# Kernel tuning notes

Measured on AMD Instinct MI355X. Metric: run time of the kernel, lower is better.

Reference implementation:

```python
import jax, jax.numpy as jnp
import numpy as np

TK, HA = 3, 8          # num_blocks, num_heads
AVGF = 32              # num_submatrices
LN_EPS = 1e-5


def _layernorm(x, g, b):
    m = jnp.mean(x, axis=-1, keepdims=True)
    v = jnp.mean((x - m) ** 2, axis=-1, keepdims=True)
    return (x - m) / jnp.sqrt(v + LN_EPS) * g + b


def setup_inputs() -> dict:
    key = jax.random.key(0)
    ks = jax.random.split(key, 12)
    A, B, T = 16, 128, 512
    M = A * B              # 2048
    Dh = M // HA           # 256
    H = 4 * M              # 8192
    s = 0.05               # scale randn params so activations stay finite
    return {
        "x": jax.random.normal(ks[0], (A, B, T), jnp.float32),
        "weight": jax.random.normal(ks[1], (M, M), jnp.float32) * s,
        "Wq": jax.random.normal(ks[2], (TK, HA, Dh, M), jnp.float32) * s,
        "Wk": jax.random.normal(ks[3], (TK, HA, Dh, M), jnp.float32) * s,
        "Wv": jax.random.normal(ks[4], (TK, HA, Dh, M), jnp.float32) * s,
        "Wo": jax.random.normal(ks[5], (TK, M, M), jnp.float32) * s,
        "ln1_g": jnp.ones((M,), jnp.float32),
        "ln1_b": jnp.zeros((M,), jnp.float32),
        "ln2_g": jnp.ones((M,), jnp.float32),
        "ln2_b": jnp.zeros((M,), jnp.float32),
        "fc1_w": jax.random.normal(ks[6], (H, M), jnp.float32) * 0.02,
        "fc1_b": jnp.zeros((H,), jnp.float32),
        "fc2_w": jax.random.normal(ks[7], (M, H), jnp.float32) * 0.02,
        "fc2_b": jnp.zeros((M,), jnp.float32),
    }


def reference(x, weight, Wq, Wk, Wv, Wo, ln1_g, ln1_b, ln2_g, ln2_b,
              fc1_w, fc1_b, fc2_w, fc2_b):
    A, B, T = x.shape
    M = A * B
    Dh = M // HA
    seg = T // AVGF
    # redefine(): transpose(0,2) -> (T,B,A), segment-average along time, flatten
    xt = jnp.transpose(x, (2, 1, 0))                       # (T, B, A)
    xc = xt.reshape(AVGF, seg, B, A).mean(axis=1)          # (AVGF, B, A)
    xcf = xc.reshape(AVGF, M)                              # (AVGF, M)
    # savespace[i] = weight @ x[i]  + sinusoidal positional bias
    pos = jnp.arange(AVGF, dtype=jnp.float32)[:, None]
    je = jnp.arange(0, M, 2, dtype=jnp.float32)
    ang = pos / (10000.0 ** (2.0 * je / M))                # (AVGF, M/2)
    bias = jnp.zeros((AVGF, M), jnp.float32)
    bias = bias.at[:, 0::2].set(jnp.sin(ang)).at[:, 1::2].set(jnp.cos(ang))
    s0 = xcf @ weight.T + bias                             # (AVGF, M)
    scale = 1.0 / jnp.sqrt(jnp.float32(Dh))

    # Sequential recurrence over tokens: vcum[a] carries the cumulative
    # softmax-weighted V sum (softmax over a scalar == 1) per block/head.
    def step(vcum, s):
        for a in range(TK):
            xn = _layernorm(s, ln1_g, ln1_b)
            q = jnp.einsum('hdm,m->hd', Wq[a], xn)         # (HA, Dh)
            k = jnp.einsum('hdm,m->hd', Wk[a], xn)
            v = jnp.einsum('hdm,m->hd', Wv[a], xn)
            scores = jnp.sum(q * k, axis=-1) * scale       # (HA,) scalars
            w = jax.nn.softmax(scores[:, None], axis=-1)[:, 0]  # ones
            vcum = vcum.at[a].add(w[:, None] * v)
            s = Wo[a] @ vcum[a].reshape(-1) + s
            s = _layernorm(s, ln2_g, ln2_b) + s
            h = jax.nn.gelu(fc1_w @ s + fc1_b, approximate=False)
            s = fc2_w @ h + fc2_b
        return vcum, s

    vcum0 = jnp.zeros((TK, HA, Dh), s0.dtype)
    _, out = jax.lax.scan(step, vcum0, s0)                 # (AVGF, M)
    return out.reshape(AVGF, B, A)
```

## Files before the change

kernel.cpp:

```cpp
#include <hip/hip_runtime.h>
#include <hip/hip_bf16.h>
#include <math.h>

typedef __attribute__((ext_vector_type(8))) short short8;
typedef __attribute__((ext_vector_type(4))) float floatx4;

__device__ inline unsigned f2bf1(float f) {
    union { float f; unsigned u; } v; v.f = f;
    return (v.u + 0x8000u) >> 16;
}

__device__ inline short8 pack8(float4 a, float4 b) {
    short8 r;
    r[0] = (short)f2bf1(a.x); r[1] = (short)f2bf1(a.y);
    r[2] = (short)f2bf1(a.z); r[3] = (short)f2bf1(a.w);
    r[4] = (short)f2bf1(b.x); r[5] = (short)f2bf1(b.y);
    r[6] = (short)f2bf1(b.z); r[7] = (short)f2bf1(b.w);
    return r;
}

__global__ __launch_bounds__(128) void avg_k(const float* __restrict__ x,
                                             float* __restrict__ xcf) {
    int blk = blockIdx.x;
    int a = blk >> 7, b = blk & 127;
    int t = threadIdx.x;
    const float4 v = *(const float4*)(x + ((size_t)a * 128 + b) * 512 + t * 4);
    float s = v.x + v.y + v.z + v.w;
    s += __shfl_xor(s, 1);
    s += __shfl_xor(s, 2);
    if ((t & 3) == 0) {
        int seg = t >> 2;
        xcf[seg * 2048 + b * 16 + a] = s * (1.0f / 16.0f);
    }
}

__global__ __launch_bounds__(256) void ln_k(const float* __restrict__ Sin,
                                            const float* __restrict__ g,
                                            const float* __restrict__ b,
                                            float* __restrict__ out, int addres) {
    __shared__ float red[8];
    const int row = blockIdx.x, t = threadIdx.x;
    const float* xr = Sin + (size_t)row * 2048;
    float4 v0 = *(const float4*)(xr + t * 4);
    float4 v1 = *(const float4*)(xr + 1024 + t * 4);
    float s = v0.x + v0.y + v0.z + v0.w + v1.x + v1.y + v1.z + v1.w;
    for (int o = 32; o; o >>= 1) s += __shfl_down(s, o);
    if ((t & 63) == 0) red[t >> 6] = s;
    __syncthreads();
    float mean = (red[0] + red[1] + red[2] + red[3]) * (1.0f / 2048.0f);
    float d0 = v0.x - mean, d1 = v0.y - mean, d2 = v0.z - mean, d3 = v0.w - mean;
    float e0 = v1.x - mean, e1 = v1.y - mean, e2 = v1.z - mean, e3 = v1.w - mean;
    float s2 = d0*d0 + d1*d1 + d2*d2 + d3*d3 + e0*e0 + e1*e1 + e2*e2 + e3*e3;
    for (int o = 32; o; o >>= 1) s2 += __shfl_down(s2, o);
    if ((t & 63) == 0) red[4 + (t >> 6)] = s2;
    __syncthreads();
    float var = (red[4] + red[5] + red[6] + red[7]) * (1.0f / 2048.0f);
    float rs = 1.0f / sqrtf(var + 1e-5f);
    float4 g0 = *(const float4*)(g + t * 4);
    float4 g1 = *(const float4*)(g + 1024 + t * 4);
    float4 b0 = *(const float4*)(b + t * 4);
    float4 b1 = *(const float4*)(b + 1024 + t * 4);
    float4 o0, o1;
    o0.x = d0 * rs * g0.x + b0.x; o0.y = d1 * rs * g0.y + b0.y;
    o0.z = d2 * rs * g0.z + b0.z; o0.w = d3 * rs * g0.w + b0.w;
    o1.x = e0 * rs * g1.x + b1.x; o1.y = e1 * rs * g1.y + b1.y;
    o1.z = e2 * rs * g1.z + b1.z; o1.w = e3 * rs * g1.w + b1.w;
    if (addres) {
        o0.x += v0.x; o0.y += v0.y; o0.z += v0.z; o0.w += v0.w;
        o1.x += v1.x; o1.y += v1.y; o1.z += v1.z; o1.w += v1.w;
    }
    *(float4*)(out + (size_t)row * 2048 + t * 4) = o0;
    *(float4*)(out + (size_t)row * 2048 + 1024 + t * 4) = o1;
}

__global__ __launch_bounds__(256) void cumsum_k(float* __restrict__ V) {
    int c = blockIdx.x * 256 + threadIdx.x;
    float run = 0.f;
#pragma unroll
    for (int i = 0; i < 32; i++) { run += V[i * 2048 + c]; V[i * 2048 + c] = run; }
}

__global__ __launch_bounds__(256) void gelu_k(float* __restrict__ H,
                                              const float* __restrict__ b1) {
    int idx4 = blockIdx.x * 256 + threadIdx.x;
    int col4 = idx4 & 2047;
    float4 v = *(const float4*)(H + (size_t)idx4 * 4);
    const float4 bb = *(const float4*)(b1 + col4 * 4);
    v.x += bb.x; v.y += bb.y; v.z += bb.z; v.w += bb.w;
    v.x = 0.5f * v.x * (1.0f + erff(v.x * 0.70710678118654752f));
    v.y = 0.5f * v.y * (1.0f + erff(v.y * 0.70710678118654752f));
    v.z = 0.5f * v.z * (1.0f + erff(v.z * 0.70710678118654752f));
    v.w = 0.5f * v.w * (1.0f + erff(v.w * 0.70710678118654752f));
    *(float4*)(H + (size_t)idx4 * 4) = v;
}

template<int KCHUNK, int MODE>
__global__ __launch_bounds__(256) void gemm_k(const float* __restrict__ X,
                                              const float* __restrict__ W,
                                              float* __restrict__ C,
                                              const float* __restrict__ bias,
                                              int N, int K) {
    constexpr int PITCH = KCHUNK + 8;
    __shared__ unsigned short Xs[32 * PITCH];
    const int tid = threadIdx.x;
    const int bx = blockIdx.x, by = blockIdx.y;
    const int kb0 = by * KCHUNK;

    constexpr int NF4 = 32 * (KCHUNK / 4);
    for (int f = tid; f < NF4; f += 256) {
        int row = f / (KCHUNK / 4), c4 = f % (KCHUNK / 4);
        const float4 v = *(const float4*)(X + (size_t)row * K + kb0 + c4 * 4);
        ushort4 p;
        p.x = (unsigned short)f2bf1(v.x);
        p.y = (unsigned short)f2bf1(v.y);
        p.z = (unsigned short)f2bf1(v.z);
        p.w = (unsigned short)f2bf1(v.w);
        *(ushort4*)&Xs[row * PITCH + c4 * 4] = p;
    }
    __syncthreads();

    const int w = tid >> 6, lane = tid & 63;
    const int q = lane >> 4, r16 = lane & 15;
    const int nb = bx * 128 + w * 32;
    floatx4 acc[2][2] = {};
    const float* wp0 = W + (size_t)(nb + r16) * K + kb0 + q * 8;
    const float* wp1 = W + (size_t)(nb + 16 + r16) * K + kb0 + q * 8;

#pragma unroll
    for (int kk = 0; kk < KCHUNK; kk += 32) {
        short8 a0 = *(const short8*)&Xs[r16 * PITCH + kk + q * 8];
        short8 a1 = *(const short8*)&Xs[(16 + r16) * PITCH + kk + q * 8];
        {
            float4 u0 = *(const float4*)(wp0 + kk);
            float4 u1 = *(const float4*)(wp0 + kk + 4);
            short8 bf = pack8(u0, u1);
            acc[0][0] = __builtin_amdgcn_mfma_f32_16x16x32_bf16(a0, bf, acc[0][0], 0, 0, 0);
            acc[1][0] = __builtin_amdgcn_mfma_f32_16x16x32_bf16(a1, bf, acc[1][0], 0, 0, 0);
        }
        {
            float4 u0 = *(const float4*)(wp1 + kk);
            float4 u1 = *(const float4*)(wp1 + kk + 4);
            short8 bf = pack8(u0, u1);
            acc[0][1] = __builtin_amdgcn_mfma_f32_16x16x32_bf16(a0, bf, acc[0][1], 0, 0, 0);
            acc[1][1] = __builtin_amdgcn_mfma_f32_16x16x32_bf16(a1, bf, acc[1][1], 0, 0, 0);
        }
    }

#pragma unroll
    for (int mt = 0; mt < 2; mt++)
#pragma unroll
        for (int nt = 0; nt < 2; nt++)
#pragma unroll
            for (int e = 0; e < 4; e++) {
                int i = mt * 16 + q * 4 + e;
                int n = nb + nt * 16 + r16;
                float v = acc[mt][nt][e];
                if (MODE == 1 && by == 0) v += bias[n];
                if (MODE == 2 && by == 0) {
                    int ne = n & ~1;
                    float ang = (float)i * __expf(-(float)ne * (9.210340371976184f / 1024.0f));
                    v += (n & 1) ? cosf(ang) : sinf(ang);
                }
                atomicAdd(C + (size_t)i * N + n, v);
            }
}

extern "C" void kernel_launch(void* const* d_in, const int* in_sizes, int n_in,
                              void* d_out, int out_size, void* d_ws, size_t ws_size,
                              hipStream_t stream) {
    const float* x      = (const float*)d_in[0];
    const float* weight = (const float*)d_in[1];
    const float* Wv     = (const float*)d_in[4];
    const float* Wo     = (const float*)d_in[5];
    const float* ln1g   = (const float*)d_in[6];
    const float* ln1b   = (const float*)d_in[7];
    const float* ln2g   = (const float*)d_in[8];
    const float* ln2b   = (const float*)d_in[9];
    const float* fc1w   = (const float*)d_in[10];
    const float* fc1b   = (const float*)d_in[11];
    const float* fc2w   = (const float*)d_in[12];
    const float* fc2b   = (const float*)d_in[13];
    float* ws  = (float*)d_ws;
    float* xcf = ws;
    float* S   = ws + 65536;
    float* Xn  = ws + 131072;
    float* V   = ws + 196608;
    float* H   = ws + 262144;
    float* out = (float*)d_out;

    avg_k<<<2048, 128, 0, stream>>>(x, xcf);

    hipMemsetAsync(S, 0, 65536 * 4, stream);
    gemm_k<128, 2><<<dim3(16, 16), 256, 0, stream>>>(xcf, weight, S, nullptr, 2048, 2048);

    for (int a = 0; a < 3; a++) {
        ln_k<<<32, 256, 0, stream>>>(S, ln1g, ln1b, Xn, 0);
        hipMemsetAsync(V, 0, 65536 * 4, stream);
        gemm_k<128, 0><<<dim3(16, 16), 256, 0, stream>>>(Xn, Wv + (size_t)a * 4194304, V, nullptr, 2048, 2048);
        cumsum_k<<<8, 256, 0, stream>>>(V);
        gemm_k<128, 0><<<dim3(16, 16), 256, 0, stream>>>(V, Wo + (size_t)a * 4194304, S, nullptr, 2048, 2048);
        ln_k<<<32, 256, 0, stream>>>(S, ln2g, ln2b, S, 1);
        hipMemsetAsync(H, 0, 262144 * 4, stream);
        gemm_k<256, 0><<<dim3(64, 8), 256, 0, stream>>>(S, fc1w, H, nullptr, 8192, 2048);
        gelu_k<<<256, 256, 0, stream>>>(H, fc1b);
        float* Co = (a == 2) ? out : S;
        hipMemsetAsync(Co, 0, 65536 * 4, stream);
        gemm_k<256, 1><<<dim3(16, 32), 256, 0, stream>>>(H, fc2w, Co, fc2b, 2048, 8192);
    }
}
```

Baseline: 494.7 us.

## Replace atomic split-K accumulation with slab partials and fused reduction epilogues

Split-K GEMMs now write their partial tiles to a per-K-chunk slab with plain stores instead of atomicAdd into memset buffers. Dedicated reduction kernels sum the partials and fuse the following elementwise work: positional bias with LN1, cumsum, residual with LN2, bias with GELU, and bias with the next block's LN1. This removes the memsets, the atomic contention, and the separate ln/cumsum/gelu passes. The cost is extra slab traffic and reduction reads, and the 2048x2048 GEMMs move to finer K-chunks (64), which doubles the split count.

Result: slower. 505.1 us (+2.1%).

```diff
diff --git a/kernel.cpp b/kernel.cpp
--- a/kernel.cpp
+++ b/kernel.cpp
@@ -34,71 +34,10 @@
     }
 }
 
-__global__ __launch_bounds__(256) void ln_k(const float* __restrict__ Sin,
-                                            const float* __restrict__ g,
-                                            const float* __restrict__ b,
-                                            float* __restrict__ out, int addres) {
-    __shared__ float red[8];
-    const int row = blockIdx.x, t = threadIdx.x;
-    const float* xr = Sin + (size_t)row * 2048;
-    float4 v0 = *(const float4*)(xr + t * 4);
-    float4 v1 = *(const float4*)(xr + 1024 + t * 4);
-    float s = v0.x + v0.y + v0.z + v0.w + v1.x + v1.y + v1.z + v1.w;
-    for (int o = 32; o; o >>= 1) s += __shfl_down(s, o);
-    if ((t & 63) == 0) red[t >> 6] = s;
-    __syncthreads();
-    float mean = (red[0] + red[1] + red[2] + red[3]) * (1.0f / 2048.0f);
-    float d0 = v0.x - mean, d1 = v0.y - mean, d2 = v0.z - mean, d3 = v0.w - mean;
-    float e0 = v1.x - mean, e1 = v1.y - mean, e2 = v1.z - mean, e3 = v1.w - mean;
-    float s2 = d0*d0 + d1*d1 + d2*d2 + d3*d3 + e0*e0 + e1*e1 + e2*e2 + e3*e3;
-    for (int o = 32; o; o >>= 1) s2 += __shfl_down(s2, o);
-    if ((t & 63) == 0) red[4 + (t >> 6)] = s2;
-    __syncthreads();
-    float var = (red[4] + red[5] + red[6] + red[7]) * (1.0f / 2048.0f);
-    float rs = 1.0f / sqrtf(var + 1e-5f);
-    float4 g0 = *(const float4*)(g + t * 4);
-    float4 g1 = *(const float4*)(g + 1024 + t * 4);
-    float4 b0 = *(const float4*)(b + t * 4);
-    float4 b1 = *(const float4*)(b + 1024 + t * 4);
-    float4 o0, o1;
-    o0.x = d0 * rs * g0.x + b0.x; o0.y = d1 * rs * g0.y + b0.y;
-    o0.z = d2 * rs * g0.z + b0.z; o0.w = d3 * rs * g0.w + b0.w;
-    o1.x = e0 * rs * g1.x + b1.x; o1.y = e1 * rs * g1.y + b1.y;
-    o1.z = e2 * rs * g1.z + b1.z; o1.w = e3 * rs * g1.w + b1.w;
-    if (addres) {
-        o0.x += v0.x; o0.y += v0.y; o0.z += v0.z; o0.w += v0.w;
-        o1.x += v1.x; o1.y += v1.y; o1.z += v1.z; o1.w += v1.w;
-    }
-    *(float4*)(out + (size_t)row * 2048 + t * 4) = o0;
-    *(float4*)(out + (size_t)row * 2048 + 1024 + t * 4) = o1;
-}
-
-__global__ __launch_bounds__(256) void cumsum_k(float* __restrict__ V) {
-    int c = blockIdx.x * 256 + threadIdx.x;
-    float run = 0.f;
-#pragma unroll
-    for (int i = 0; i < 32; i++) { run += V[i * 2048 + c]; V[i * 2048 + c] = run; }
-}
-
-__global__ __launch_bounds__(256) void gelu_k(float* __restrict__ H,
-                                              const float* __restrict__ b1) {
-    int idx4 = blockIdx.x * 256 + threadIdx.x;
-    int col4 = idx4 & 2047;
-    float4 v = *(const float4*)(H + (size_t)idx4 * 4);
-    const float4 bb = *(const float4*)(b1 + col4 * 4);
-    v.x += bb.x; v.y += bb.y; v.z += bb.z; v.w += bb.w;
-    v.x = 0.5f * v.x * (1.0f + erff(v.x * 0.70710678118654752f));
-    v.y = 0.5f * v.y * (1.0f + erff(v.y * 0.70710678118654752f));
-    v.z = 0.5f * v.z * (1.0f + erff(v.z * 0.70710678118654752f));
-    v.w = 0.5f * v.w * (1.0f + erff(v.w * 0.70710678118654752f));
-    *(float4*)(H + (size_t)idx4 * 4) = v;
-}
-
-template<int KCHUNK, int MODE>
+template<int KCHUNK>
 __global__ __launch_bounds__(256) void gemm_k(const float* __restrict__ X,
                                               const float* __restrict__ W,
-                                              float* __restrict__ C,
-                                              const float* __restrict__ bias,
+                                              float* __restrict__ slab,
                                               int N, int K) {
     constexpr int PITCH = KCHUNK + 8;
     __shared__ unsigned short Xs[32 * PITCH];
@@ -107,6 +46,7 @@
     const int kb0 = by * KCHUNK;
 
     constexpr int NF4 = 32 * (KCHUNK / 4);
+#pragma unroll
     for (int f = tid; f < NF4; f += 256) {
         int row = f / (KCHUNK / 4), c4 = f % (KCHUNK / 4);
         const float4 v = *(const float4*)(X + (size_t)row * K + kb0 + c4 * 4);
@@ -146,6 +86,7 @@
         }
     }
 
+    float* outp = slab + (size_t)by * 32 * N;
 #pragma unroll
     for (int mt = 0; mt < 2; mt++)
 #pragma unroll
@@ -154,15 +95,183 @@
             for (int e = 0; e < 4; e++) {
                 int i = mt * 16 + q * 4 + e;
                 int n = nb + nt * 16 + r16;
-                float v = acc[mt][nt][e];
-                if (MODE == 1 && by == 0) v += bias[n];
-                if (MODE == 2 && by == 0) {
-                    int ne = n & ~1;
-                    float ang = (float)i * __expf(-(float)ne * (9.210340371976184f / 1024.0f));
-                    v += (n & 1) ? cosf(ang) : sinf(ang);
-                }
-                atomicAdd(C + (size_t)i * N + n, v);
+                outp[(size_t)i * N + n] = acc[mt][nt][e];
             }
+}
+
+template<int NCH>
+__device__ inline float4 csum4(const float* __restrict__ slab, size_t stride, size_t off) {
+    float4 a; a.x = 0.f; a.y = 0.f; a.z = 0.f; a.w = 0.f;
+#pragma unroll 8
+    for (int c = 0; c < NCH; c++) {
+        const float4 v = *(const float4*)(slab + (size_t)c * stride + off);
+        a.x += v.x; a.y += v.y; a.z += v.z; a.w += v.w;
+    }
+    return a;
+}
+
+__device__ inline float block_sum(float v, float* red, int t) {
+    for (int o = 32; o; o >>= 1) v += __shfl_down(v, o);
+    if ((t & 63) == 0) red[t >> 6] = v;
+    __syncthreads();
+    float r = red[0] + red[1] + red[2] + red[3];
+    __syncthreads();
+    return r;
+}
+
+#define KEXP (-9.210340371976184f / 1024.0f)
+
+__global__ __launch_bounds__(256) void rW_k(const float* __restrict__ slab,
+                                            const float* __restrict__ g,
+                                            const float* __restrict__ bl,
+                                            float* __restrict__ S,
+                                            float* __restrict__ Xn) {
+    __shared__ float red[4];
+    const int row = blockIdx.x, t = threadIdx.x;
+    const size_t off0 = (size_t)row * 2048 + t * 4, off1 = off0 + 1024;
+    float4 v0 = csum4<32>(slab, 65536, off0);
+    float4 v1 = csum4<32>(slab, 65536, off1);
+    const float fr = (float)row;
+    const int c0 = t * 4, c1 = c0 + 1024;
+    float a0 = fr * __expf((float)c0 * KEXP);
+    float a1 = fr * __expf((float)(c0 + 2) * KEXP);
+    float a2 = fr * __expf((float)c1 * KEXP);
+    float a3 = fr * __expf((float)(c1 + 2) * KEXP);
+    v0.x += sinf(a0); v0.y += cosf(a0); v0.z += sinf(a1); v0.w += cosf(a1);
+    v1.x += sinf(a2); v1.y += cosf(a2); v1.z += sinf(a3); v1.w += cosf(a3);
+    *(float4*)(S + off0) = v0;
+    *(float4*)(S + off1) = v1;
+    float s = v0.x + v0.y + v0.z + v0.w + v1.x + v1.y + v1.z + v1.w;
+    float mean = block_sum(s, red, t) * (1.0f / 2048.0f);
+    float d0 = v0.x - mean, d1 = v0.y - mean, d2 = v0.z - mean, d3 = v0.w - mean;
+    float e0 = v1.x - mean, e1 = v1.y - mean, e2 = v1.z - mean, e3 = v1.w - mean;
+    float s2 = d0*d0 + d1*d1 + d2*d2 + d3*d3 + e0*e0 + e1*e1 + e2*e2 + e3*e3;
+    float var = block_sum(s2, red, t) * (1.0f / 2048.0f);
+    float rs = 1.0f / sqrtf(var + 1e-5f);
+    float4 g0 = *(const float4*)(g + c0), g1 = *(const float4*)(g + c1);
+    float4 b0 = *(const float4*)(bl + c0), b1 = *(const float4*)(bl + c1);
+    float4 o0, o1;
+    o0.x = d0 * rs * g0.x + b0.x; o0.y = d1 * rs * g0.y + b0.y;
+    o0.z = d2 * rs * g0.z + b0.z; o0.w = d3 * rs * g0.w + b0.w;
+    o1.x = e0 * rs * g1.x + b1.x; o1.y = e1 * rs * g1.y + b1.y;
+    o1.z = e2 * rs * g1.z + b1.z; o1.w = e3 * rs * g1.w + b1.w;
+    *(float4*)(Xn + off0) = o0;
+    *(float4*)(Xn + off1) = o1;
+}
+
+__global__ __launch_bounds__(256) void rVcum_k(const float* __restrict__ slab,
+                                               float* __restrict__ Vc) {
+    __shared__ float lds[32 * 64];
+    const int b = blockIdx.x, t = threadIdx.x;
+    {
+        int row = t >> 4, c4 = t & 15;
+        size_t off = (size_t)row * 2048 + b * 64 + c4 * 4;
+        float4 v = csum4<32>(slab, 65536, off);
+        *(float4*)&lds[row * 64 + c4 * 4] = v;
+    }
+    {
+        int row = (t >> 4) + 16, c4 = t & 15;
+        size_t off = (size_t)row * 2048 + b * 64 + c4 * 4;
+        float4 v = csum4<32>(slab, 65536, off);
+        *(float4*)&lds[row * 64 + c4 * 4] = v;
+    }
+    __syncthreads();
+    if (t < 64) {
+        float run = 0.f;
+#pragma unroll
+        for (int i = 0; i < 32; i++) {
+            run += lds[i * 64 + t];
+            Vc[(size_t)i * 2048 + b * 64 + t] = run;
+        }
+    }
+}
+
+__global__ __launch_bounds__(256) void rO_k(const float* __restrict__ slab,
+                                            const float* __restrict__ S,
+                                            const float* __restrict__ g,
+                                            const float* __restrict__ bl,
+                                            float* __restrict__ S2) {
+    __shared__ float red[4];
+    const int row = blockIdx.x, t = threadIdx.x;
+    const size_t off0 = (size_t)row * 2048 + t * 4, off1 = off0 + 1024;
+    float4 v0 = csum4<32>(slab, 65536, off0);
+    float4 v1 = csum4<32>(slab, 65536, off1);
+    const float4 s0 = *(const float4*)(S + off0);
+    const float4 s1 = *(const float4*)(S + off1);
+    v0.x += s0.x; v0.y += s0.y; v0.z += s0.z; v0.w += s0.w;
+    v1.x += s1.x; v1.y += s1.y; v1.z += s1.z; v1.w += s1.w;
+    float s = v0.x + v0.y + v0.z + v0.w + v1.x + v1.y + v1.z + v1.w;
+    float mean = block_sum(s, red, t) * (1.0f / 2048.0f);
+    float d0 = v0.x - mean, d1 = v0.y - mean, d2 = v0.z - mean, d3 = v0.w - mean;
+    float e0 = v1.x - mean, e1 = v1.y - mean, e2 = v1.z - mean, e3 = v1.w - mean;
+    float s2 = d0*d0 + d1*d1 + d2*d2 + d3*d3 + e0*e0 + e1*e1 + e2*e2 + e3*e3;
+    float var = block_sum(s2, red, t) * (1.0f / 2048.0f);
+    float rs = 1.0f / sqrtf(var + 1e-5f);
+    const int c0 = t * 4, c1 = c0 + 1024;
+    float4 g0 = *(const float4*)(g + c0), g1 = *(const float4*)(g + c1);
+    float4 b0 = *(const float4*)(bl + c0), b1 = *(const float4*)(bl + c1);
+    float4 o0, o1;
+    o0.x = d0 * rs * g0.x + b0.x + v0.x; o0.y = d1 * rs * g0.y + b0.y + v0.y;
+    o0.z = d2 * rs * g0.z + b0.z + v0.z; o0.w = d3 * rs * g0.w + b0.w + v0.w;
+    o1.x = e0 * rs * g1.x + b1.x + v1.x; o1.y = e1 * rs * g1.y + b1.y + v1.y;
+    o1.z = e2 * rs * g1.z + b1.z + v1.z; o1.w = e3 * rs * g1.w + b1.w + v1.w;
+    *(float4*)(S2 + off0) = o0;
+    *(float4*)(S2 + off1) = o1;
+}
+
+__global__ __launch_bounds__(256) void rFC1_k(const float* __restrict__ slab,
+                                              const float* __restrict__ bias,
+                                              float* __restrict__ Hb) {
+    const int row = blockIdx.x, t = threadIdx.x;
+#pragma unroll
+    for (int j = 0; j < 8; j++) {
+        const int c4 = t + 256 * j;
+        const size_t off = (size_t)row * 8192 + c4 * 4;
+        float4 v = csum4<8>(slab, 262144, off);
+        const float4 bb = *(const float4*)(bias + c4 * 4);
+        v.x += bb.x; v.y += bb.y; v.z += bb.z; v.w += bb.w;
+        v.x = 0.5f * v.x * (1.0f + erff(v.x * 0.70710678118654752f));
+        v.y = 0.5f * v.y * (1.0f + erff(v.y * 0.70710678118654752f));
+        v.z = 0.5f * v.z * (1.0f + erff(v.z * 0.70710678118654752f));
+        v.w = 0.5f * v.w * (1.0f + erff(v.w * 0.70710678118654752f));
+        *(float4*)(Hb + off) = v;
+    }
+}
+
+__global__ __launch_bounds__(256) void rFC2_k(const float* __restrict__ slab,
+                                              const float* __restrict__ bias,
+                                              float* __restrict__ Sdst,
+                                              float* __restrict__ Xn,
+                                              const float* __restrict__ g,
+                                              const float* __restrict__ bl) {
+    __shared__ float red[4];
+    const int row = blockIdx.x, t = threadIdx.x;
+    const size_t off0 = (size_t)row * 2048 + t * 4, off1 = off0 + 1024;
+    const int c0 = t * 4, c1 = c0 + 1024;
+    float4 v0 = csum4<32>(slab, 65536, off0);
+    float4 v1 = csum4<32>(slab, 65536, off1);
+    const float4 bb0 = *(const float4*)(bias + c0);
+    const float4 bb1 = *(const float4*)(bias + c1);
+    v0.x += bb0.x; v0.y += bb0.y; v0.z += bb0.z; v0.w += bb0.w;
+    v1.x += bb1.x; v1.y += bb1.y; v1.z += bb1.z; v1.w += bb1.w;
+    *(float4*)(Sdst + off0) = v0;
+    *(float4*)(Sdst + off1) = v1;
+    float s = v0.x + v0.y + v0.z + v0.w + v1.x + v1.y + v1.z + v1.w;
+    float mean = block_sum(s, red, t) * (1.0f / 2048.0f);
+    float d0 = v0.x - mean, d1 = v0.y - mean, d2 = v0.z - mean, d3 = v0.w - mean;
+    float e0 = v1.x - mean, e1 = v1.y - mean, e2 = v1.z - mean, e3 = v1.w - mean;
+    float s2 = d0*d0 + d1*d1 + d2*d2 + d3*d3 + e0*e0 + e1*e1 + e2*e2 + e3*e3;
+    float var = block_sum(s2, red, t) * (1.0f / 2048.0f);
+    float rs = 1.0f / sqrtf(var + 1e-5f);
+    float4 g0 = *(const float4*)(g + c0), g1 = *(const float4*)(g + c1);
+    float4 b0 = *(const float4*)(bl + c0), b1 = *(const float4*)(bl + c1);
+    float4 o0, o1;
+    o0.x = d0 * rs * g0.x + b0.x; o0.y = d1 * rs * g0.y + b0.y;
+    o0.z = d2 * rs * g0.z + b0.z; o0.w = d3 * rs * g0.w + b0.w;
+    o1.x = e0 * rs * g1.x + b1.x; o1.y = e1 * rs * g1.y + b1.y;
+    o1.z = e2 * rs * g1.z + b1.z; o1.w = e3 * rs * g1.w + b1.w;
+    *(float4*)(Xn + off0) = o0;
+    *(float4*)(Xn + off1) = o1;
 }
 
 extern "C" void kernel_launch(void* const* d_in, const int* in_sizes, int n_in,
@@ -180,31 +289,29 @@
     const float* fc1b   = (const float*)d_in[11];
     const float* fc2w   = (const float*)d_in[12];
     const float* fc2b   = (const float*)d_in[13];
-    float* ws  = (float*)d_ws;
-    float* xcf = ws;
-    float* S   = ws + 65536;
-    float* Xn  = ws + 131072;
-    float* V   = ws + 196608;
-    float* H   = ws + 262144;
-    float* out = (float*)d_out;
+    float* ws   = (float*)d_ws;
+    float* xcf  = ws;
+    float* S    = ws + 65536;
+    float* Xn   = ws + 131072;
+    float* S2   = ws + 196608;
+    float* Vc   = ws + 262144;
+    float* Hb   = ws + 327680;
+    float* slab = ws + 589824;
+    float* out  = (float*)d_out;
 
     avg_k<<<2048, 128, 0, stream>>>(x, xcf);
 
-    hipMemsetAsync(S, 0, 65536 * 4, stream);
-    gemm_k<128, 2><<<dim3(16, 16), 256, 0, stream>>>(xcf, weight, S, nullptr, 2048, 2048);
+    gemm_k<64><<<dim3(16, 32), 256, 0, stream>>>(xcf, weight, slab, 2048, 2048);
+    rW_k<<<32, 256, 0, stream>>>(slab, ln1g, ln1b, S, Xn);
 
     for (int a = 0; a < 3; a++) {
-        ln_k<<<32, 256, 0, stream>>>(S, ln1g, ln1b, Xn, 0);
-        hipMemsetAsync(V, 0, 65536 * 4, stream);
-        gemm_k<128, 0><<<dim3(16, 16), 256, 0, stream>>>(Xn, Wv + (size_t)a * 4194304, V, nullptr, 2048, 2048);
-        cumsum_k<<<8, 256, 0, stream>>>(V);
-        gemm_k<128, 0><<<dim3(16, 16), 256, 0, stream>>>(V, Wo + (size_t)a * 4194304, S, nullptr, 2048, 2048);
-        ln_k<<<32, 256, 0, stream>>>(S, ln2g, ln2b, S, 1);
-        hipMemsetAsync(H, 0, 262144 * 4, stream);
-        gemm_k<256, 0><<<dim3(64, 8), 256, 0, stream>>>(S, fc1w, H, nullptr, 8192, 2048);
-        gelu_k<<<256, 256, 0, stream>>>(H, fc1b);
-        float* Co = (a == 2) ? out : S;
-        hipMemsetAsync(Co, 0, 65536 * 4, stream);
-        gemm_k<256, 1><<<dim3(16, 32), 256, 0, stream>>>(H, fc2w, Co, fc2b, 2048, 8192);
-    }
-}
+        gemm_k<64><<<dim3(16, 32), 256, 0, stream>>>(Xn, Wv + (size_t)a * 4194304, slab, 2048, 2048);
+        rVcum_k<<<32, 256, 0, stream>>>(slab, Vc);
+        gemm_k<64><<<dim3(16, 32), 256, 0, stream>>>(Vc, Wo + (size_t)a * 4194304, slab, 2048, 2048);
+        rO_k<<<32, 256, 0, stream>>>(slab, S, ln2g, ln2b, S2);
+        gemm_k<256><<<dim3(64, 8), 256, 0, stream>>>(S2, fc1w, slab, 8192, 2048);
+        rFC1_k<<<32, 256, 0, stream>>>(slab, fc1b, Hb);
+        gemm_k<256><<<dim3(16, 32), 256, 0, stream>>>(Hb, fc2w, slab, 2048, 8192);
+        rFC2_k<<<32, 256, 0, stream>>>(slab, fc2b, (a == 2) ? out : S, Xn, ln1g, ln1b);
+    }
+}
```

## Replace atomic split-K with slab reduction kernels and fuse layernorm into GEMM prologue

Applied to the files above, without the earlier changes.

The split-K GEMMs now write partial results to a slab buffer instead of using atomicAdd. Separate reduction kernels sum those partials and fuse in the bias, positional encoding, residual, GELU and cumsum, and they also emit per-row sum and sum-of-squares. The following GEMM applies layernorm in its X-load prologue from those statistics, which removes the standalone ln_k, cumsum, gelu and memset launches. K chunks are also halved to give more blocks. The cost is extra slab memory traffic, and the single-pass variance (E[x²]−mean²) carries some risk of numerical cancellation.

After: 516.6 us. 1.04x slower.

```diff
diff --git a/kernel.cpp b/kernel.cpp
--- a/kernel.cpp
+++ b/kernel.cpp
@@ -4,6 +4,8 @@
 
 typedef __attribute__((ext_vector_type(8))) short short8;
 typedef __attribute__((ext_vector_type(4))) float floatx4;
+
+#define KEXP (-9.210340371976184f / 1024.0f)
 
 __device__ inline unsigned f2bf1(float f) {
     union { float f; unsigned u; } v; v.f = f;
@@ -34,88 +36,65 @@
     }
 }
 
-__global__ __launch_bounds__(256) void ln_k(const float* __restrict__ Sin,
-                                            const float* __restrict__ g,
-                                            const float* __restrict__ b,
-                                            float* __restrict__ out, int addres) {
-    __shared__ float red[8];
-    const int row = blockIdx.x, t = threadIdx.x;
-    const float* xr = Sin + (size_t)row * 2048;
-    float4 v0 = *(const float4*)(xr + t * 4);
-    float4 v1 = *(const float4*)(xr + 1024 + t * 4);
-    float s = v0.x + v0.y + v0.z + v0.w + v1.x + v1.y + v1.z + v1.w;
-    for (int o = 32; o; o >>= 1) s += __shfl_down(s, o);
-    if ((t & 63) == 0) red[t >> 6] = s;
-    __syncthreads();
-    float mean = (red[0] + red[1] + red[2] + red[3]) * (1.0f / 2048.0f);
-    float d0 = v0.x - mean, d1 = v0.y - mean, d2 = v0.z - mean, d3 = v0.w - mean;
-    float e0 = v1.x - mean, e1 = v1.y - mean, e2 = v1.z - mean, e3 = v1.w - mean;
-    float s2 = d0*d0 + d1*d1 + d2*d2 + d3*d3 + e0*e0 + e1*e1 + e2*e2 + e3*e3;
-    for (int o = 32; o; o >>= 1) s2 += __shfl_down(s2, o);
-    if ((t & 63) == 0) red[4 + (t >> 6)] = s2;
-    __syncthreads();
-    float var = (red[4] + red[5] + red[6] + red[7]) * (1.0f / 2048.0f);
-    float rs = 1.0f / sqrtf(var + 1e-5f);
-    float4 g0 = *(const float4*)(g + t * 4);
-    float4 g1 = *(const float4*)(g + 1024 + t * 4);
-    float4 b0 = *(const float4*)(b + t * 4);
-    float4 b1 = *(const float4*)(b + 1024 + t * 4);
-    float4 o0, o1;
-    o0.x = d0 * rs * g0.x + b0.x; o0.y = d1 * rs * g0.y + b0.y;
-    o0.z = d2 * rs * g0.z + b0.z; o0.w = d3 * rs * g0.w + b0.w;
-    o1.x = e0 * rs * g1.x + b1.x; o1.y = e1 * rs * g1.y + b1.y;
-    o1.z = e2 * rs * g1.z + b1.z; o1.w = e3 * rs * g1.w + b1.w;
-    if (addres) {
-        o0.x += v0.x; o0.y += v0.y; o0.z += v0.z; o0.w += v0.w;
-        o1.x += v1.x; o1.y += v1.y; o1.z += v1.z; o1.w += v1.w;
-    }
-    *(float4*)(out + (size_t)row * 2048 + t * 4) = o0;
-    *(float4*)(out + (size_t)row * 2048 + 1024 + t * 4) = o1;
-}
-
-__global__ __launch_bounds__(256) void cumsum_k(float* __restrict__ V) {
-    int c = blockIdx.x * 256 + threadIdx.x;
-    float run = 0.f;
-#pragma unroll
-    for (int i = 0; i < 32; i++) { run += V[i * 2048 + c]; V[i * 2048 + c] = run; }
-}
-
-__global__ __launch_bounds__(256) void gelu_k(float* __restrict__ H,
-                                              const float* __restrict__ b1) {
-    int idx4 = blockIdx.x * 256 + threadIdx.x;
-    int col4 = idx4 & 2047;
-    float4 v = *(const float4*)(H + (size_t)idx4 * 4);
-    const float4 bb = *(const float4*)(b1 + col4 * 4);
-    v.x += bb.x; v.y += bb.y; v.z += bb.z; v.w += bb.w;
-    v.x = 0.5f * v.x * (1.0f + erff(v.x * 0.70710678118654752f));
-    v.y = 0.5f * v.y * (1.0f + erff(v.y * 0.70710678118654752f));
-    v.z = 0.5f * v.z * (1.0f + erff(v.z * 0.70710678118654752f));
-    v.w = 0.5f * v.w * (1.0f + erff(v.w * 0.70710678118654752f));
-    *(float4*)(H + (size_t)idx4 * 4) = v;
-}
-
-template<int KCHUNK, int MODE>
+template<int KCHUNK, int XMODE>
 __global__ __launch_bounds__(256) void gemm_k(const float* __restrict__ X,
                                               const float* __restrict__ W,
-                                              float* __restrict__ C,
-                                              const float* __restrict__ bias,
+                                              float* __restrict__ slab,
+                                              const float* __restrict__ g,
+                                              const float* __restrict__ bl,
+                                              const float* __restrict__ psum,
+                                              const float* __restrict__ psq,
                                               int N, int K) {
     constexpr int PITCH = KCHUNK + 8;
     __shared__ unsigned short Xs[32 * PITCH];
+    __shared__ float ldsM[32], ldsR[32];
     const int tid = threadIdx.x;
     const int bx = blockIdx.x, by = blockIdx.y;
     const int kb0 = by * KCHUNK;
 
-    constexpr int NF4 = 32 * (KCHUNK / 4);
-    for (int f = tid; f < NF4; f += 256) {
+    constexpr int PER = (32 * (KCHUNK / 4)) / 256;
+    float4 xv[PER], gv[PER], bv[PER];
+    int rows[PER], c4s[PER];
+#pragma unroll
+    for (int p = 0; p < PER; p++) {
+        int f = tid + 256 * p;
         int row = f / (KCHUNK / 4), c4 = f % (KCHUNK / 4);
-        const float4 v = *(const float4*)(X + (size_t)row * K + kb0 + c4 * 4);
-        ushort4 p;
-        p.x = (unsigned short)f2bf1(v.x);
-        p.y = (unsigned short)f2bf1(v.y);
-        p.z = (unsigned short)f2bf1(v.z);
-        p.w = (unsigned short)f2bf1(v.w);
-        *(ushort4*)&Xs[row * PITCH + c4 * 4] = p;
+        rows[p] = row; c4s[p] = c4;
+        xv[p] = *(const float4*)(X + (size_t)row * K + kb0 + c4 * 4);
+        if (XMODE != 0) {
+            gv[p] = *(const float4*)(g + kb0 + c4 * 4);
+            bv[p] = *(const float4*)(bl + kb0 + c4 * 4);
+        }
+    }
+    if (XMODE != 0 && tid < 32) {
+        float s = 0.f, q = 0.f;
+#pragma unroll
+        for (int j = 0; j < 8; j++) { s += psum[tid * 8 + j]; q += psq[tid * 8 + j]; }
+        float mean = s * (1.0f / 2048.0f);
+        float var = q * (1.0f / 2048.0f) - mean * mean;
+        ldsM[tid] = mean;
+        ldsR[tid] = rsqrtf(var + 1e-5f);
+    }
+    __syncthreads();
+#pragma unroll
+    for (int p = 0; p < PER; p++) {
+        float4 v = xv[p];
+        if (XMODE != 0) {
+            float m = ldsM[rows[p]], r = ldsR[rows[p]];
+            float4 o;
+            o.x = (v.x - m) * r * gv[p].x + bv[p].x;
+            o.y = (v.y - m) * r * gv[p].y + bv[p].y;
+            o.z = (v.z - m) * r * gv[p].z + bv[p].z;
+            o.w = (v.w - m) * r * gv[p].w + bv[p].w;
+            if (XMODE == 2) { o.x += v.x; o.y += v.y; o.z += v.z; o.w += v.w; }
+            v = o;
+        }
+        ushort4 pk;
+        pk.x = (unsigned short)f2bf1(v.x);
+        pk.y = (unsigned short)f2bf1(v.y);
+        pk.z = (unsigned short)f2bf1(v.z);
+        pk.w = (unsigned short)f2bf1(v.w);
+        *(ushort4*)&Xs[rows[p] * PITCH + c4s[p] * 4] = pk;
     }
     __syncthreads();
 
@@ -146,6 +125,7 @@
         }
     }
 
+    float* outp = slab + (size_t)by * 32 * N;
 #pragma unroll
     for (int mt = 0; mt < 2; mt++)
 #pragma unroll
@@ -154,15 +134,86 @@
             for (int e = 0; e < 4; e++) {
                 int i = mt * 16 + q * 4 + e;
                 int n = nb + nt * 16 + r16;
-                float v = acc[mt][nt][e];
-                if (MODE == 1 && by == 0) v += bias[n];
-                if (MODE == 2 && by == 0) {
-                    int ne = n & ~1;
-                    float ang = (float)i * __expf(-(float)ne * (9.210340371976184f / 1024.0f));
-                    v += (n & 1) ? cosf(ang) : sinf(ang);
-                }
-                atomicAdd(C + (size_t)i * N + n, v);
+                outp[(size_t)i * N + n] = acc[mt][nt][e];
             }
+}
+
+template<int NCH, int MODE>
+__global__ __launch_bounds__(256) void red_k(const float* __restrict__ slab,
+                                             const float* __restrict__ bias,
+                                             float* __restrict__ dst,
+                                             float* __restrict__ psum,
+                                             float* __restrict__ psq) {
+    __shared__ float rs[4], rq[4];
+    const int b = blockIdx.x, t = threadIdx.x;
+    const int row = b >> 3, cg = b & 7;
+    const int col = cg * 256 + t;
+    const size_t off = (size_t)row * 2048 + col;
+    float v = 0.f;
+#pragma unroll
+    for (int c = 0; c < NCH; c++) v += slab[(size_t)c * 65536 + off];
+    if (MODE == 0) {
+        int ne = col & ~1;
+        float ang = (float)row * __expf((float)ne * KEXP);
+        v += (col & 1) ? cosf(ang) : sinf(ang);
+    } else if (MODE == 1) {
+        v += dst[off];
+    } else {
+        v += bias[col];
+    }
+    dst[off] = v;
+    float s = v, q = v * v;
+    for (int o = 32; o; o >>= 1) { s += __shfl_down(s, o); q += __shfl_down(q, o); }
+    if ((t & 63) == 0) { rs[t >> 6] = s; rq[t >> 6] = q; }
+    __syncthreads();
+    if (t == 0) {
+        psum[row * 8 + cg] = rs[0] + rs[1] + rs[2] + rs[3];
+        psq[row * 8 + cg]  = rq[0] + rq[1] + rq[2] + rq[3];
+    }
+}
+
+__global__ __launch_bounds__(256) void rVcum_k(const float* __restrict__ slab,
+                                               float* __restrict__ Vc) {
+    __shared__ float lds[256];
+    const int cgBase = blockIdx.x * 8;
+    const int t = threadIdx.x;
+    const int row = t >> 3, c = t & 7;
+    const size_t off = (size_t)row * 2048 + cgBase + c;
+    float v = 0.f;
+#pragma unroll
+    for (int ch = 0; ch < 32; ch++) v += slab[(size_t)ch * 65536 + off];
+    lds[row * 8 + c] = v;
+    __syncthreads();
+    if (t < 8) {
+        float run = 0.f;
+#pragma unroll
+        for (int i = 0; i < 32; i++) {
+            run += lds[i * 8 + t];
+            Vc[(size_t)i * 2048 + cgBase + t] = run;
+        }
+    }
+}
+
+__global__ __launch_bounds__(256) void rFC1_k(const float* __restrict__ slab,
+                                              const float* __restrict__ bias,
+                                              float* __restrict__ Hb) {
+    const int b = blockIdx.x, t = threadIdx.x;
+    const int row = b >> 3, cg = b & 7;
+    const int c4 = cg * 256 + t;
+    const size_t off = (size_t)row * 8192 + c4 * 4;
+    float4 v; v.x = 0.f; v.y = 0.f; v.z = 0.f; v.w = 0.f;
+#pragma unroll
+    for (int c = 0; c < 16; c++) {
+        const float4 u = *(const float4*)(slab + (size_t)c * 262144 + off);
+        v.x += u.x; v.y += u.y; v.z += u.z; v.w += u.w;
+    }
+    const float4 bb = *(const float4*)(bias + c4 * 4);
+    v.x += bb.x; v.y += bb.y; v.z += bb.z; v.w += bb.w;
+    v.x = 0.5f * v.x * (1.0f + erff(v.x * 0.70710678118654752f));
+    v.y = 0.5f * v.y * (1.0f + erff(v.y * 0.70710678118654752f));
+    v.z = 0.5f * v.z * (1.0f + erff(v.z * 0.70710678118654752f));
+    v.w = 0.5f * v.w * (1.0f + erff(v.w * 0.70710678118654752f));
+    *(float4*)(Hb + off) = v;
 }
 
 extern "C" void kernel_launch(void* const* d_in, const int* in_sizes, int n_in,
@@ -180,31 +231,34 @@
     const float* fc1b   = (const float*)d_in[11];
     const float* fc2w   = (const float*)d_in[12];
     const float* fc2b   = (const float*)d_in[13];
-    float* ws  = (float*)d_ws;
-    float* xcf = ws;
-    float* S   = ws + 65536;
-    float* Xn  = ws + 131072;
-    float* V   = ws + 196608;
-    float* H   = ws + 262144;
-    float* out = (float*)d_out;
+    float* ws   = (float*)d_ws;
+    float* xcf  = ws;
+    float* S    = ws + 65536;
+    float* Vc   = ws + 131072;
+    float* Hb   = ws + 196608;
+    float* psum = ws + 458752;
+    float* psq  = ws + 459008;
+    float* slab = ws + 460800;
+    float* out  = (float*)d_out;
 
     avg_k<<<2048, 128, 0, stream>>>(x, xcf);
 
-    hipMemsetAsync(S, 0, 65536 * 4, stream);
-    gemm_k<128, 2><<<dim3(16, 16), 256, 0, stream>>>(xcf, weight, S, nullptr, 2048, 2048);
+    gemm_k<64, 0><<<dim3(16, 32), 256, 0, stream>>>(xcf, weight, slab,
+        nullptr, nullptr, nullptr, nullptr, 2048, 2048);
+    red_k<32, 0><<<256, 256, 0, stream>>>(slab, nullptr, S, psum, psq);
 
     for (int a = 0; a < 3; a++) {
-        ln_k<<<32, 256, 0, stream>>>(S, ln1g, ln1b, Xn, 0);
-        hipMemsetAsync(V, 0, 65536 * 4, stream);
-        gemm_k<128, 0><<<dim3(16, 16), 256, 0, stream>>>(Xn, Wv + (size_t)a * 4194304, V, nullptr, 2048, 2048);
-        cumsum_k<<<8, 256, 0, stream>>>(V);
-        gemm_k<128, 0><<<dim3(16, 16), 256, 0, stream>>>(V, Wo + (size_t)a * 4194304, S, nullptr, 2048, 2048);
-        ln_k<<<32, 256, 0, stream>>>(S, ln2g, ln2b, S, 1);
-        hipMemsetAsync(H, 0, 262144 * 4, stream);
-        gemm_k<256, 0><<<dim3(64, 8), 256, 0, stream>>>(S, fc1w, H, nullptr, 8192, 2048);
-        gelu_k<<<256, 256, 0, stream>>>(H, fc1b);
-        float* Co = (a == 2) ? out : S;
-        hipMemsetAsync(Co, 0, 65536 * 4, stream);
-        gemm_k<256, 1><<<dim3(16, 32), 256, 0, stream>>>(H, fc2w, Co, fc2b, 2048, 8192);
-    }
-}
+        gemm_k<64, 1><<<dim3(16, 32), 256, 0, stream>>>(S, Wv + (size_t)a * 4194304,
+            slab, ln1g, ln1b, psum, psq, 2048, 2048);
+        rVcum_k<<<256, 256, 0, stream>>>(slab, Vc);
+        gemm_k<64, 0><<<dim3(16, 32), 256, 0, stream>>>(Vc, Wo + (size_t)a * 4194304,
+            slab, nullptr, nullptr, nullptr, nullptr, 2048, 2048);
+        red_k<32, 1><<<256, 256, 0, stream>>>(slab, nullptr, S, psum, psq);
+        gemm_k<128, 2><<<dim3(64, 16), 256, 0, stream>>>(S, fc1w, slab,
+            ln2g, ln2b, psum, psq, 8192, 2048);
+        rFC1_k<<<256, 256, 0, stream>>>(slab, fc1b, Hb);
+        gemm_k<128, 0><<<dim3(16, 64), 256, 0, stream>>>(Hb, fc2w, slab,
+            nullptr, nullptr, nullptr, nullptr, 2048, 8192);
+        red_k<64, 2><<<256, 256, 0, stream>>>(slab, fc2b, (a == 2) ? out : S, psum, psq);
+    }
+}
```
